# Performance work log

Measured on AMD Instinct MI355X. Metric: run time of the kernel, lower is better.

The kernel has to match this reference:

```python
import jax, jax.numpy as jnp
import numpy as np

B, S, D = 2, 2048, 1024
QH, KVH, DH = 16, 4, 64
TOP_K = 128
ROPE_BASE = 10000.0


def _rope(x):
    # x: [B, H, S, DH]; standard LLaMA-style rotate-half RoPE, no freq scaling
    half = DH // 2
    inv_freq = 1.0 / (ROPE_BASE ** (jnp.arange(half, dtype=jnp.float32) / half))
    ang = jnp.arange(S, dtype=jnp.float32)[:, None] * inv_freq[None, :]  # [S, half]
    cos, sin = jnp.cos(ang), jnp.sin(ang)
    x1, x2 = x[..., :half], x[..., half:]
    return jnp.concatenate([x1 * cos - x2 * sin, x2 * cos + x1 * sin], axis=-1)


def setup_inputs() -> dict:
    key = jax.random.key(0)
    ks = jax.random.split(key, 5)
    return {
        "x": jax.random.normal(ks[0], (B, S, D), dtype=jnp.float32),
        "Wq": jax.random.normal(ks[1], (QH * DH, D), dtype=jnp.float32) * 0.02,
        "Wk": jax.random.normal(ks[2], (KVH * DH, D), dtype=jnp.float32) * 0.02,
        "Wv": jax.random.normal(ks[3], (KVH * DH, D), dtype=jnp.float32) * 0.02,
        "Wo": jax.random.normal(ks[4], (D, QH * DH), dtype=jnp.float32) * 0.02,
    }


def reference(x, Wq, Wk, Wv, Wo):
    # projections (Linear, no bias): y = x @ W.T
    q = (x @ Wq.T).reshape(B, S, QH, DH).transpose(0, 2, 1, 3)   # [B,QH,S,DH]
    k = (x @ Wk.T).reshape(B, S, KVH, DH).transpose(0, 2, 1, 3)  # [B,KVH,S,DH]
    v = (x @ Wv.T).reshape(B, S, KVH, DH).transpose(0, 2, 1, 3)
    q = _rope(q)
    k = _rope(k)
    # repeat_kv: GQA expand kv heads to q heads
    rep = QH // KVH
    k = jnp.repeat(k, rep, axis=1)
    v = jnp.repeat(v, rep, axis=1)
    scores = jnp.einsum("bhqd,bhkd->bhqk", q, k) / np.sqrt(DH)  # [B,QH,S,S]
    causal = jnp.triu(jnp.ones((S, S), dtype=bool), k=1)
    scores = jnp.where(causal, -jnp.inf, scores)
    # top-k masking before softmax: keep entries >= per-row k-th largest score
    top_vals = jax.lax.top_k(scores, TOP_K)[0]        # [B,QH,S,TOP_K]
    thr = top_vals[..., -1:]
    scores = jnp.where(scores < thr, -jnp.inf, scores)
    w = jax.nn.softmax(scores, axis=-1)
    out = jnp.einsum("bhqk,bhkd->bhqd", w, v)         # [B,QH,S,DH]
    out = out.transpose(0, 2, 1, 3).reshape(B, S, QH * DH)
    return out @ Wo.T
```

## Files before the change

kernel.cpp:

```cpp
#include <hip/hip_runtime.h>
#include <hip/hip_bf16.h>
#include <hip/hip_fp16.h>
#include <math.h>

constexpr int cB   = 2;
constexpr int cS   = 2048;
constexpr int cD   = 1024;
constexpr int cQH  = 16;
constexpr int cKVH = 4;
constexpr int cDH  = 64;
constexpr int cTOPK = 128;
constexpr int cM   = cB * cS;
constexpr int cNB  = cS / 64;
constexpr int cLSZ = 384;

constexpr int cTI  = 8;
constexpr int cSTR = 130;

constexpr int cNQ  = cQH * cDH;
constexpr int cNK  = cKVH * cDH;
constexpr int cNQKV = cNQ + 2 * cNK;

typedef __attribute__((ext_vector_type(8))) short short8;
typedef __attribute__((ext_vector_type(4))) float floatx4;
typedef _Float16 half8 __attribute__((ext_vector_type(8)));

__device__ inline ushort f2bf(float f) {
    unsigned u = __float_as_uint(f);
    return (ushort)((u + 0x7FFFu + ((u >> 16) & 1u)) >> 16);
}

__device__ __forceinline__ void glds16(const ushort* g, ushort* l) {
    __builtin_amdgcn_global_load_lds(
        (const __attribute__((address_space(1))) unsigned int*)g,
        (__attribute__((address_space(3))) unsigned int*)l, 16, 0, 0);
}

constexpr int cE0 = cM * cD;
constexpr int cE1 = cE0 + cNQ * cD;
constexpr int cE2 = cE1 + cNK * cD;
constexpr int cE3 = cE2 + cNK * cD;
constexpr int cE4 = cE3 + cD * cQH * cDH;

__global__ void cast_all_bf16(const float* __restrict__ x,
                              const float* __restrict__ wq,
                              const float* __restrict__ wk,
                              const float* __restrict__ wv,
                              const float* __restrict__ wo,
                              ushort* __restrict__ dst) {
    const int i4 = (blockIdx.x * blockDim.x + threadIdx.x) * 4;
    if (i4 >= cE4) return;
    const float* s;
    int off;
    if (i4 < cE0)      { s = x;  off = i4; }
    else if (i4 < cE1) { s = wq; off = i4 - cE0; }
    else if (i4 < cE2) { s = wk; off = i4 - cE1; }
    else if (i4 < cE3) { s = wv; off = i4 - cE2; }
    else               { s = wo; off = i4 - cE3; }
    const float4 v = *(const float4*)(s + off);
    ushort4 r;
    r.x = f2bf(v.x); r.y = f2bf(v.y); r.z = f2bf(v.z); r.w = f2bf(v.w);
    *(ushort4*)(dst + i4) = r;
}

__global__ __launch_bounds__(256) void gemm_bf16_bt(
        const ushort* __restrict__ A, const ushort* __restrict__ W,
        float* __restrict__ C, int M, int N, int K) {
    __shared__ ushort AsL[128 * 32];
    __shared__ ushort BsL[128 * 32];

    const int tid  = threadIdx.x;
    const int lane = tid & 63;
    const int w    = tid >> 6;
    const int wm   = (w & 1) * 64;
    const int wn   = (w >> 1) * 64;
    const int m0   = blockIdx.y * 128;
    const int n0   = blockIdx.x * 128;
    const int quad = lane >> 4;
    const int l16  = lane & 15;

    int r0, q0, r1, q1;
    {
        const int g5 = (w * 128 + lane) & 31;
        const int b4 = (g5 >> 4) & 1, b3 = (g5 >> 3) & 1, b2 = (g5 >> 2) & 1;
        const int b1 = (g5 >> 1) & 1, b0 = g5 & 1;
        r0 = ((w * 128 + lane) >> 5) * 8 + ((b4 << 2) | (b3 << 1) | (b2 ^ b4));
        q0 = ((b1 ^ b3) << 1) | (b0 ^ b2 ^ b4);
    }
    {
        const int gI = w * 128 + 64 + lane;
        const int g5 = gI & 31;
        const int b4 = (g5 >> 4) & 1, b3 = (g5 >> 3) & 1, b2 = (g5 >> 2) & 1;
        const int b1 = (g5 >> 1) & 1, b0 = g5 & 1;
        r1 = (gI >> 5) * 8 + ((b4 << 2) | (b3 << 1) | (b2 ^ b4));
        q1 = ((b1 ^ b3) << 1) | (b0 ^ b2 ^ b4);
    }
    const size_t aOff0 = (size_t)(m0 + r0) * K + q0 * 8;
    const size_t aOff1 = (size_t)(m0 + r1) * K + q1 * 8;
    const size_t bOff0 = (size_t)(n0 + r0) * K + q0 * 8;
    const size_t bOff1 = (size_t)(n0 + r1) * K + q1 * 8;
    ushort* ldsA0 = AsL + w * 1024;
    ushort* ldsA1 = AsL + w * 1024 + 512;
    ushort* ldsB0 = BsL + w * 1024;
    ushort* ldsB1 = BsL + w * 1024 + 512;

    int eA[4], eB[4];
    #pragma unroll
    for (int mi = 0; mi < 4; ++mi) {
        const int rr = wm + mi * 16 + l16;
        eA[mi] = (((rr >> 3) * 32) + ((4 * (rr & 7) + quad) ^ (rr & 7))) * 8;
    }
    #pragma unroll
    for (int ni = 0; ni < 4; ++ni) {
        const int rn = wn + ni * 16 + l16;
        eB[ni] = (((rn >> 3) * 32) + ((4 * (rn & 7) + quad) ^ (rn & 7))) * 8;
    }

    floatx4 acc[4][4];
    #pragma unroll
    for (int mi = 0; mi < 4; ++mi)
        #pragma unroll
        for (int ni = 0; ni < 4; ++ni)
            acc[mi][ni] = (floatx4){0.f, 0.f, 0.f, 0.f};

    for (int k0 = 0; k0 < K; k0 += 32) {
        glds16(A + aOff0 + k0, ldsA0);
        glds16(A + aOff1 + k0, ldsA1);
        glds16(W + bOff0 + k0, ldsB0);
        glds16(W + bOff1 + k0, ldsB1);
        __syncthreads();

        short8 af[4], bf[4];
        #pragma unroll
        for (int mi = 0; mi < 4; ++mi)
            af[mi] = *(const short8*)(AsL + eA[mi]);
        #pragma unroll
        for (int ni = 0; ni < 4; ++ni)
            bf[ni] = *(const short8*)(BsL + eB[ni]);
        #pragma unroll
        for (int mi = 0; mi < 4; ++mi)
            #pragma unroll
            for (int ni = 0; ni < 4; ++ni)
                acc[mi][ni] = __builtin_amdgcn_mfma_f32_16x16x32_bf16(
                    af[mi], bf[ni], acc[mi][ni], 0, 0, 0);
        __syncthreads();
    }

    #pragma unroll
    for (int mi = 0; mi < 4; ++mi)
        #pragma unroll
        for (int ni = 0; ni < 4; ++ni)
            #pragma unroll
            for (int r = 0; r < 4; ++r) {
                const int row = m0 + wm + mi * 16 + quad * 4 + r;
                const int col = n0 + wn + ni * 16 + l16;
                C[(size_t)row * N + col] = acc[mi][ni][r];
            }
}

__global__ void rope_cast_f16(const float* __restrict__ src,
                              ushort* __restrict__ dst, int H, int total,
                              float scale, int srcStride) {
    int idx = blockIdx.x * blockDim.x + threadIdx.x;
    if (idx >= total) return;
    const int d   = idx & 31;
    const int h   = (idx >> 5) % H;
    const int row = idx / (32 * H);
    const int s   = row % cS;
    const float inv_freq = powf(10000.0f, -(float)d / 32.0f);
    const float ang = (float)s * inv_freq;
    const float c  = cosf(ang);
    const float si = sinf(ang);
    const float* p = src + (size_t)row * srcStride + (size_t)h * cDH;
    const float x1 = p[d];
    const float x2 = p[d + 32];
    const float r1 = (x1 * c - x2 * si) * scale;
    const float r2 = (x2 * c + x1 * si) * scale;
    ushort* o = dst + (size_t)row * H * cDH + (size_t)h * cDH;
    o[d]      = __builtin_bit_cast(ushort, (_Float16)r1);
    o[d + 32] = __builtin_bit_cast(ushort, (_Float16)r2);
}

__global__ void cast_f32_f16_strided(const float* __restrict__ src,
                                     ushort* __restrict__ dst,
                                     int total, int cols, int srcStride) {
    const int i4 = (blockIdx.x * blockDim.x + threadIdx.x) * 4;
    if (i4 >= total) return;
    const int row = i4 / cols;
    const int col = i4 - row * cols;
    const float4 v = *(const float4*)(src + (size_t)row * srcStride + col);
    ushort4 r;
    r.x = __builtin_bit_cast(ushort, (_Float16)v.x);
    r.y = __builtin_bit_cast(ushort, (_Float16)v.y);
    r.z = __builtin_bit_cast(ushort, (_Float16)v.z);
    r.w = __builtin_bit_cast(ushort, (_Float16)v.w);
    *(ushort4*)(dst + i4) = r;
}

__device__ inline unsigned fmap(float f) {
    unsigned u = __float_as_uint(f);
    return (u & 0x80000000u) ? ~u : (u | 0x80000000u);
}
__device__ inline float funmap(unsigned u) {
    unsigned v = (u & 0x80000000u) ? (u & 0x7FFFFFFFu) : ~u;
    return __uint_as_float(v);
}

__global__ __launch_bounds__(512) void attn_tile_kernel(
        const ushort* __restrict__ qf, const ushort* __restrict__ kf,
        const ushort* __restrict__ vf, ushort* __restrict__ out) {
    extern __shared__ char smem[];
    unsigned* stg = (unsigned*)smem;
    unsigned* klA = (unsigned*)smem;
    int*      jlA = (int*)(klA + cTI * cLSZ);

    const int lane = threadIdx.x & 63;
    const int wv   = __builtin_amdgcn_readfirstlane(threadIdx.x >> 6);

    const int x  = blockIdx.x;
    const int it = (cS / cTI - 1) - (x >> 5);
    const int bh = x & 31;
    const int h  = bh & 15;
    const int b  = bh >> 4;
    const int kvh = h >> 2;
    const int i0  = it * cTI;

    const size_t bS = (size_t)b * cS;
    const int l16   = lane & 15;
    const int quad  = lane >> 4;
    const int jperm = ((lane & 3) << 4) + (lane >> 2);
    const int i     = i0 + wv;

    const ushort* qp = qf + ((bS + i0 + (l16 & 7)) * cQH + h) * cDH + quad * 8;
    const half8 a0h = __builtin_bit_cast(half8, *(const uint4*)qp);
    const half8 a1h = __builtin_bit_cast(half8, *(const uint4*)(qp + 32));

    unsigned key[cNB];
    #pragma unroll
    for (int jb = 0; jb < cNB; ++jb) key[jb] = 0u;

    const int nk16   = ((i0 + cTI - 1) >> 4) + 1;
    const int nchunk = (nk16 + 7) >> 3;

    uint4 pb0, pb1;
    if (wv < nk16) {
        const ushort* kp = kf + ((bS + (wv << 4) + l16) * cKVH + kvh) * cDH + quad * 8;
        pb0 = *(const uint4*)kp;
        pb1 = *(const uint4*)(kp + 32);
    }

    #pragma unroll
    for (int c = 0; c < 16; ++c) {
        if (c >= nchunk) break;
        const int  kb16  = (c << 3) + wv;
        const bool valid = (kb16 < nk16);
        const uint4 b0 = pb0, b1 = pb1;
        const int  kb16n = ((c + 1) << 3) + wv;
        if (kb16n < nk16) {
            const ushort* kp = kf + ((bS + (kb16n << 4) + l16) * cKVH + kvh) * cDH + quad * 8;
            pb0 = *(const uint4*)kp;
            pb1 = *(const uint4*)(kp + 32);
        }
        if (valid) {
            floatx4 acc = (floatx4){0.f, 0.f, 0.f, 0.f};
            acc = __builtin_amdgcn_mfma_f32_16x16x32_f16(
                a0h, __builtin_bit_cast(half8, b0), acc, 0, 0, 0);
            acc = __builtin_amdgcn_mfma_f32_16x16x32_f16(
                a1h, __builtin_bit_cast(half8, b1), acc, 0, 0, 0);
            if (quad < 2) {
                unsigned* sp = stg + (c & 1) * (cTI * cSTR) + (wv << 4) + l16;
                #pragma unroll
                for (int r2 = 0; r2 < 4; ++r2)
                    sp[(quad * 4 + r2) * cSTR] = __float_as_uint(acc[r2]);
            }
        }
        __syncthreads();
        {
            const unsigned* rp = stg + (c & 1) * (cTI * cSTR) + wv * cSTR;
            #pragma unroll
            for (int jj = 0; jj < 2; ++jj) {
                const int j = (c << 7) + (jj << 6) + jperm;
                const unsigned kr = rp[(jj << 6) + jperm];
                key[(c << 1) + jj] =
                    (j <= i) ? fmap(__uint_as_float(kr)) : 0u;
            }
        }
    }
    __syncthreads();

    const int nb = (i >> 6) + 1;
    unsigned* kl = klA + wv * cLSZ;
    int*      jl = jlA + wv * cLSZ;
    const int vbase0 = (int)(((unsigned)bS * cKVH + kvh) * cDH);

    unsigned um = 0u, un = 0xFFFFFFFFu;
    #pragma unroll
    for (int jb = 0; jb < cNB; ++jb) {
        if (jb >= nb) break;
        const unsigned kk = key[jb];
        um = max(um, kk);
        un = min(un, kk ? kk : 0xFFFFFFFFu);
    }
    #pragma unroll
    for (int off = 32; off >= 1; off >>= 1) {
        um = max(um, (unsigned)__shfl_xor((int)um, off));
        un = min(un, (unsigned)__shfl_xor((int)un, off));
    }
    const float mrow = funmap(um);

    unsigned ustar;
    if (i < cTOPK) {
        ustar = un;
    } else {
        unsigned lo = un, hi = um;
        while (lo < hi) {
            const unsigned d   = hi - lo;
            const unsigned mid = lo + (d >> 1) + (d & 1u);
            int cnt2 = 0;
            #pragma unroll
            for (int jb = 0; jb < cNB; ++jb) {
                if (jb >= nb) break;
                cnt2 += __popcll(__ballot(key[jb] >= mid));
            }
            if (cnt2 == cTOPK) {
                unsigned mn = 0xFFFFFFFFu;
                #pragma unroll
                for (int jb = 0; jb < cNB; ++jb) {
                    if (jb >= nb) break;
                    const unsigned kk = key[jb];
                    mn = min(mn, (kk >= mid) ? kk : 0xFFFFFFFFu);
                }
                #pragma unroll
                for (int off = 32; off >= 1; off >>= 1)
                    mn = min(mn, (unsigned)__shfl_xor((int)mn, off));
                lo = mn;
                break;
            }
            if (cnt2 > cTOPK) lo = mid; else hi = mid - 1u;
        }
        ustar = lo;
    }

    const unsigned long long mlt = (1ull << lane) - 1ull;
    int base = 0;
    #pragma unroll
    for (int jb = 0; jb < cNB; ++jb) {
        if (jb >= nb) break;
        const int j = (jb << 6) + jperm;
        const bool keep = (j <= i) && (key[jb] >= ustar);
        const unsigned long long mk = __ballot(keep);
        const int pos = base + __popcll(mk & mlt);
        if (keep && pos < cLSZ) {
            kl[pos] = key[jb];
            jl[pos] = vbase0 + j * (cKVH * cDH);
        }
        base += __popcll(mk);
    }
    const int cnt = min(base, cLSZ);

    float zp = 0.f;
    for (int t = lane; t < cnt; t += 64) {
        const float s  = funmap(kl[t]);
        const float wt = __expf(s - mrow);
        ((float*)kl)[t] = wt;
        zp += wt;
    }
    #pragma unroll
    for (int off = 32; off >= 1; off >>= 1) zp += __shfl_xor(zp, off);
    const float invZ = 1.0f / zp;

    float ac0 = 0.f, ac1 = 0.f, ac2 = 0.f, ac3 = 0.f;
    float ac4 = 0.f, ac5 = 0.f, ac6 = 0.f, ac7 = 0.f;
    int t = 0;
    #pragma unroll 2
    for (; t + 7 < cnt; t += 8) {
        const float wt0 = ((float*)kl)[t];
        const float wt1 = ((float*)kl)[t + 1];
        const float wt2 = ((float*)kl)[t + 2];
        const float wt3 = ((float*)kl)[t + 3];
        const float wt4 = ((float*)kl)[t + 4];
        const float wt5 = ((float*)kl)[t + 5];
        const float wt6 = ((float*)kl)[t + 6];
        const float wt7 = ((float*)kl)[t + 7];
        const int vo0 = jl[t];
        const int vo1 = jl[t + 1];
        const int vo2 = jl[t + 2];
        const int vo3 = jl[t + 3];
        const int vo4 = jl[t + 4];
        const int vo5 = jl[t + 5];
        const int vo6 = jl[t + 6];
        const int vo7 = jl[t + 7];
        ac0 += wt0 * (float)__builtin_bit_cast(_Float16, vf[vo0 + lane]);
        ac1 += wt1 * (float)__builtin_bit_cast(_Float16, vf[vo1 + lane]);
        ac2 += wt2 * (float)__builtin_bit_cast(_Float16, vf[vo2 + lane]);
        ac3 += wt3 * (float)__builtin_bit_cast(_Float16, vf[vo3 + lane]);
        ac4 += wt4 * (float)__builtin_bit_cast(_Float16, vf[vo4 + lane]);
        ac5 += wt5 * (float)__builtin_bit_cast(_Float16, vf[vo5 + lane]);
        ac6 += wt6 * (float)__builtin_bit_cast(_Float16, vf[vo6 + lane]);
        ac7 += wt7 * (float)__builtin_bit_cast(_Float16, vf[vo7 + lane]);
    }
    for (; t < cnt; ++t) {
        const float wt = ((float*)kl)[t];
        const int   vo = jl[t];
        ac0 += wt * (float)__builtin_bit_cast(_Float16, vf[vo + lane]);
    }
    const float acc = ((ac0 + ac1) + (ac2 + ac3)) + ((ac4 + ac5) + (ac6 + ac7));
    out[((bS + i) * cQH + h) * cDH + lane] = f2bf(acc * invZ);
}

extern "C" void kernel_launch(void* const* d_in, const int* in_sizes, int n_in,
                              void* d_out, int out_size, void* d_ws, size_t ws_size,
                              hipStream_t stream) {
    const float* x  = (const float*)d_in[0];
    const float* Wq = (const float*)d_in[1];
    const float* Wk = (const float*)d_in[2];
    const float* Wv = (const float*)d_in[3];
    const float* Wo = (const float*)d_in[4];
    float* out = (float*)d_out;

    float*  qkvb = (float*)d_ws;
    ushort* xh   = (ushort*)(qkvb + (size_t)cM * cNQKV);
    ushort* Wqh  = xh  + (size_t)cM * cD;
    ushort* Wkh  = Wqh + (size_t)cNQ * cD;
    ushort* Wvh  = Wkh + (size_t)cNK * cD;
    ushort* Woh  = Wvh + (size_t)cNK * cD;
    ushort* abh  = Woh + (size_t)cD * cQH * cDH;
    ushort* qff  = abh + (size_t)cM * cQH * cDH;
    ushort* kff  = qff + (size_t)cM * cQH * cDH;
    ushort* vff  = kff + (size_t)cM * cKVH * cDH;

    dim3 blk(256);

    cast_all_bf16<<<(cE4 / 4 + 255) / 256, blk, 0, stream>>>(
        x, Wq, Wk, Wv, Wo, xh);

    gemm_bf16_bt<<<dim3(cNQKV / 128, cM / 128), blk, 0, stream>>>(
        xh, Wqh, qkvb, cM, cNQKV, cD);

    {
        const int totq = cM * cQH * 32;
        const int totk = cM * cKVH * 32;
        rope_cast_f16<<<(totq + 255) / 256, blk, 0, stream>>>(
            qkvb, qff, cQH, totq, 0.125f, cNQKV);
        rope_cast_f16<<<(totk + 255) / 256, blk, 0, stream>>>(
            qkvb + cNQ, kff, cKVH, totk, 1.0f, cNQKV);
        const int nv = cM * cNK;
        cast_f32_f16_strided<<<(nv / 4 + 255) / 256, blk, 0, stream>>>(
            qkvb + cNQ + cNK, vff, nv, cNK, cNQKV);
    }

    constexpr size_t aSMEM = (size_t)cTI * cLSZ * 8;
    static_assert(2 * cTI * cSTR * 4 <= (int)aSMEM, "staging must fit");
    attn_tile_kernel<<<dim3(32 * (cS / cTI)), dim3(512), aSMEM, stream>>>(
        qff, kff, vff, abh);

    gemm_bf16_bt<<<dim3(cD / 128, cM / 128), blk, 0, stream>>>(abh, Woh, out, cM, cD, cD);
}
```

Before: 534.9 us.

## Precompute RoPE trig table, pack score/index pairs, move key mapping into MFMA store

Adds a kernel that builds cos/sin tables once per call, so the RoPE kernels look values up instead of calling powf/sinf/cosf for every element. In the attention kernel, the causal mask and float-to-orderable-key mapping now run when the MFMA results are written to shared memory. Kept weights and value offsets are packed as uint2 pairs so one LDS read fetches both. The software prefetch of K fragments for the next chunk is removed, which exposes global-load latency in the score loop. The extra launch and table reads add a little overhead.

```diff
diff --git a/kernel.cpp b/kernel.cpp
--- a/kernel.cpp
+++ b/kernel.cpp
@@ -63,6 +63,17 @@
     *(ushort4*)(dst + i4) = r;
 }
 
+__global__ void build_trig(float* __restrict__ ct, float* __restrict__ st) {
+    const int idx = blockIdx.x * blockDim.x + threadIdx.x;
+    if (idx >= cS * 32) return;
+    const int d = idx & 31;
+    const int s = idx >> 5;
+    const float inv_freq = powf(10000.0f, -(float)d / 32.0f);
+    const float ang = (float)s * inv_freq;
+    ct[idx] = cosf(ang);
+    st[idx] = sinf(ang);
+}
+
 __global__ __launch_bounds__(256) void gemm_bf16_bt(
         const ushort* __restrict__ A, const ushort* __restrict__ W,
         float* __restrict__ C, int M, int N, int K) {
@@ -160,17 +171,17 @@
 
 __global__ void rope_cast_f16(const float* __restrict__ src,
                               ushort* __restrict__ dst, int H, int total,
-                              float scale, int srcStride) {
+                              float scale, int srcStride,
+                              const float* __restrict__ ct,
+                              const float* __restrict__ st) {
     int idx = blockIdx.x * blockDim.x + threadIdx.x;
     if (idx >= total) return;
     const int d   = idx & 31;
     const int h   = (idx >> 5) % H;
     const int row = idx / (32 * H);
     const int s   = row % cS;
-    const float inv_freq = powf(10000.0f, -(float)d / 32.0f);
-    const float ang = (float)s * inv_freq;
-    const float c  = cosf(ang);
-    const float si = sinf(ang);
+    const float c  = ct[(s << 5) + d];
+    const float si = st[(s << 5) + d];
     const float* p = src + (size_t)row * srcStride + (size_t)h * cDH;
     const float x1 = p[d];
     const float x2 = p[d + 32];
@@ -210,9 +221,8 @@
         const ushort* __restrict__ qf, const ushort* __restrict__ kf,
         const ushort* __restrict__ vf, ushort* __restrict__ out) {
     extern __shared__ char smem[];
-    unsigned* stg = (unsigned*)smem;
-    unsigned* klA = (unsigned*)smem;
-    int*      jlA = (int*)(klA + cTI * cLSZ);
+    unsigned* stg  = (unsigned*)smem;
+    uint2*    kl2A = (uint2*)smem;
 
     const int lane = threadIdx.x & 63;
     const int wv   = __builtin_amdgcn_readfirstlane(threadIdx.x >> 6);
@@ -242,36 +252,27 @@
     const int nk16   = ((i0 + cTI - 1) >> 4) + 1;
     const int nchunk = (nk16 + 7) >> 3;
 
-    uint4 pb0, pb1;
-    if (wv < nk16) {
-        const ushort* kp = kf + ((bS + (wv << 4) + l16) * cKVH + kvh) * cDH + quad * 8;
-        pb0 = *(const uint4*)kp;
-        pb1 = *(const uint4*)(kp + 32);
-    }
-
     #pragma unroll
     for (int c = 0; c < 16; ++c) {
         if (c >= nchunk) break;
         const int  kb16  = (c << 3) + wv;
-        const bool valid = (kb16 < nk16);
-        const uint4 b0 = pb0, b1 = pb1;
-        const int  kb16n = ((c + 1) << 3) + wv;
-        if (kb16n < nk16) {
-            const ushort* kp = kf + ((bS + (kb16n << 4) + l16) * cKVH + kvh) * cDH + quad * 8;
-            pb0 = *(const uint4*)kp;
-            pb1 = *(const uint4*)(kp + 32);
-        }
-        if (valid) {
+        if (kb16 < nk16) {
+            const ushort* kp = kf + ((bS + (kb16 << 4) + l16) * cKVH + kvh) * cDH + quad * 8;
+            const uint4 b0 = *(const uint4*)kp;
+            const uint4 b1 = *(const uint4*)(kp + 32);
             floatx4 acc = (floatx4){0.f, 0.f, 0.f, 0.f};
             acc = __builtin_amdgcn_mfma_f32_16x16x32_f16(
                 a0h, __builtin_bit_cast(half8, b0), acc, 0, 0, 0);
             acc = __builtin_amdgcn_mfma_f32_16x16x32_f16(
                 a1h, __builtin_bit_cast(half8, b1), acc, 0, 0, 0);
             if (quad < 2) {
+                const int jg = (kb16 << 4) + l16;
                 unsigned* sp = stg + (c & 1) * (cTI * cSTR) + (wv << 4) + l16;
                 #pragma unroll
-                for (int r2 = 0; r2 < 4; ++r2)
-                    sp[(quad * 4 + r2) * cSTR] = __float_as_uint(acc[r2]);
+                for (int r2 = 0; r2 < 4; ++r2) {
+                    const int qrow = quad * 4 + r2;
+                    sp[qrow * cSTR] = (jg <= i0 + qrow) ? fmap(acc[r2]) : 0u;
+                }
             }
         }
         __syncthreads();
@@ -281,16 +282,14 @@
             for (int jj = 0; jj < 2; ++jj) {
                 const int j = (c << 7) + (jj << 6) + jperm;
                 const unsigned kr = rp[(jj << 6) + jperm];
-                key[(c << 1) + jj] =
-                    (j <= i) ? fmap(__uint_as_float(kr)) : 0u;
+                key[(c << 1) + jj] = (j <= i) ? kr : 0u;
             }
         }
     }
     __syncthreads();
 
     const int nb = (i >> 6) + 1;
-    unsigned* kl = klA + wv * cLSZ;
-    int*      jl = jlA + wv * cLSZ;
+    uint2* kl = kl2A + wv * cLSZ;
     const int vbase0 = (int)(((unsigned)bS * cKVH + kvh) * cDH);
 
     unsigned um = 0u, un = 0xFFFFFFFFu;
@@ -351,8 +350,10 @@
         const unsigned long long mk = __ballot(keep);
         const int pos = base + __popcll(mk & mlt);
         if (keep && pos < cLSZ) {
-            kl[pos] = key[jb];
-            jl[pos] = vbase0 + j * (cKVH * cDH);
+            uint2 e;
+            e.x = key[jb];
+            e.y = (unsigned)(vbase0 + j * (cKVH * cDH));
+            kl[pos] = e;
         }
         base += __popcll(mk);
     }
@@ -360,9 +361,9 @@
 
     float zp = 0.f;
     for (int t = lane; t < cnt; t += 64) {
-        const float s  = funmap(kl[t]);
+        const float s  = funmap(kl[t].x);
         const float wt = __expf(s - mrow);
-        ((float*)kl)[t] = wt;
+        kl[t].x = __float_as_uint(wt);
         zp += wt;
     }
     #pragma unroll
@@ -374,35 +375,26 @@
     int t = 0;
     #pragma unroll 2
     for (; t + 7 < cnt; t += 8) {
-        const float wt0 = ((float*)kl)[t];
-        const float wt1 = ((float*)kl)[t + 1];
-        const float wt2 = ((float*)kl)[t + 2];
-        const float wt3 = ((float*)kl)[t + 3];
-        const float wt4 = ((float*)kl)[t + 4];
-        const float wt5 = ((float*)kl)[t + 5];
-        const float wt6 = ((float*)kl)[t + 6];
-        const float wt7 = ((float*)kl)[t + 7];
-        const int vo0 = jl[t];
-        const int vo1 = jl[t + 1];
-        const int vo2 = jl[t + 2];
-        const int vo3 = jl[t + 3];
-        const int vo4 = jl[t + 4];
-        const int vo5 = jl[t + 5];
-        const int vo6 = jl[t + 6];
-        const int vo7 = jl[t + 7];
-        ac0 += wt0 * (float)__builtin_bit_cast(_Float16, vf[vo0 + lane]);
-        ac1 += wt1 * (float)__builtin_bit_cast(_Float16, vf[vo1 + lane]);
-        ac2 += wt2 * (float)__builtin_bit_cast(_Float16, vf[vo2 + lane]);
-        ac3 += wt3 * (float)__builtin_bit_cast(_Float16, vf[vo3 + lane]);
-        ac4 += wt4 * (float)__builtin_bit_cast(_Float16, vf[vo4 + lane]);
-        ac5 += wt5 * (float)__builtin_bit_cast(_Float16, vf[vo5 + lane]);
-        ac6 += wt6 * (float)__builtin_bit_cast(_Float16, vf[vo6 + lane]);
-        ac7 += wt7 * (float)__builtin_bit_cast(_Float16, vf[vo7 + lane]);
+        const uint2 e0 = kl[t];
+        const uint2 e1 = kl[t + 1];
+        const uint2 e2 = kl[t + 2];
+        const uint2 e3 = kl[t + 3];
+        const uint2 e4 = kl[t + 4];
+        const uint2 e5 = kl[t + 5];
+        const uint2 e6 = kl[t + 6];
+        const uint2 e7 = kl[t + 7];
+        ac0 += __uint_as_float(e0.x) * (float)__builtin_bit_cast(_Float16, vf[(int)e0.y + lane]);
+        ac1 += __uint_as_float(e1.x) * (float)__builtin_bit_cast(_Float16, vf[(int)e1.y + lane]);
+        ac2 += __uint_as_float(e2.x) * (float)__builtin_bit_cast(_Float16, vf[(int)e2.y + lane]);
+        ac3 += __uint_as_float(e3.x) * (float)__builtin_bit_cast(_Float16, vf[(int)e3.y + lane]);
+        ac4 += __uint_as_float(e4.x) * (float)__builtin_bit_cast(_Float16, vf[(int)e4.y + lane]);
+        ac5 += __uint_as_float(e5.x) * (float)__builtin_bit_cast(_Float16, vf[(int)e5.y + lane]);
+        ac6 += __uint_as_float(e6.x) * (float)__builtin_bit_cast(_Float16, vf[(int)e6.y + lane]);
+        ac7 += __uint_as_float(e7.x) * (float)__builtin_bit_cast(_Float16, vf[(int)e7.y + lane]);
     }
     for (; t < cnt; ++t) {
-        const float wt = ((float*)kl)[t];
-        const int   vo = jl[t];
-        ac0 += wt * (float)__builtin_bit_cast(_Float16, vf[vo + lane]);
+        const uint2 e = kl[t];
+        ac0 += __uint_as_float(e.x) * (float)__builtin_bit_cast(_Float16, vf[(int)e.y + lane]);
     }
     const float acc = ((ac0 + ac1) + (ac2 + ac3)) + ((ac4 + ac5) + (ac6 + ac7));
     out[((bS + i) * cQH + h) * cDH + lane] = f2bf(acc * invZ);
@@ -428,11 +420,15 @@
     ushort* qff  = abh + (size_t)cM * cQH * cDH;
     ushort* kff  = qff + (size_t)cM * cQH * cDH;
     ushort* vff  = kff + (size_t)cM * cKVH * cDH;
+    float*  ct   = (float*)(vff + (size_t)cM * cKVH * cDH);
+    float*  st   = ct + (size_t)cS * 32;
 
     dim3 blk(256);
 
     cast_all_bf16<<<(cE4 / 4 + 255) / 256, blk, 0, stream>>>(
         x, Wq, Wk, Wv, Wo, xh);
+
+    build_trig<<<(cS * 32 + 255) / 256, blk, 0, stream>>>(ct, st);
 
     gemm_bf16_bt<<<dim3(cNQKV / 128, cM / 128), blk, 0, stream>>>(
         xh, Wqh, qkvb, cM, cNQKV, cD);
@@ -441,9 +437,9 @@
         const int totq = cM * cQH * 32;
         const int totk = cM * cKVH * 32;
         rope_cast_f16<<<(totq + 255) / 256, blk, 0, stream>>>(
-            qkvb, qff, cQH, totq, 0.125f, cNQKV);
+            qkvb, qff, cQH, totq, 0.125f, cNQKV, ct, st);
         rope_cast_f16<<<(totk + 255) / 256, blk, 0, stream>>>(
-            qkvb + cNQ, kff, cKVH, totk, 1.0f, cNQKV);
+            qkvb + cNQ, kff, cKVH, totk, 1.0f, cNQKV, ct, st);
         const int nv = cM * cNK;
         cast_f32_f16_strided<<<(nv / 4 + 255) / 256, blk, 0, stream>>>(
             qkvb + cNQ + cNK, vff, nv, cNK, cNQKV);
```

New measurement: 535.4 us. About the same (+0.1%).
